# Performance work log

Hardware: AMD Instinct MI355X
Metric: run time of the kernel (lower is better)

The kernel has to match this reference:

```python
import jax, jax.numpy as jnp
import numpy as np

N = 4096      # number of nodes (tokens)
U = 128       # units (feature dim)
E = 131072    # number of edges (avg degree 32)


def _sage(x, src, dst, W_l, b_l, W_r):
    """PyG SAGEConv with mean aggregation.
    out = lin_l(mean_{j->i} x_j) + lin_r(x_i); lin_l has bias, lin_r does not.
    """
    n = x.shape[0]
    agg = jax.ops.segment_sum(x[src], dst, num_segments=n)
    deg = jax.ops.segment_sum(jnp.ones((src.shape[0],), x.dtype), dst, num_segments=n)
    agg = agg / jnp.maximum(deg, 1.0)[:, None]  # nodes w/o in-edges -> 0
    return agg @ W_l.T + b_l + x @ W_r.T


def setup_inputs() -> dict:
    key = jax.random.key(0)
    ks = jax.random.split(key, 20)
    s = 1.0 / np.sqrt(U)
    inp = {
        "x": jax.random.normal(ks[0], (N, U), jnp.float32),
        "edge_index": jax.random.randint(ks[1], (2, E), 0, N, jnp.int64),
        "batch": jnp.zeros((N,), jnp.int64),
        # conv_first
        "Wf_l": jax.random.normal(ks[2], (U, U), jnp.float32) * s,
        "bf_l": jnp.zeros((U,), jnp.float32),
        "Wf_r": jax.random.normal(ks[3], (U, U), jnp.float32) * s,
        # conv_common[0]
        "Wcm_l": jax.random.normal(ks[4], (U, U), jnp.float32) * s,
        "bcm_l": jnp.zeros((U,), jnp.float32),
        "Wcm_r": jax.random.normal(ks[5], (U, U), jnp.float32) * s,
        # conv_actor[0]
        "Wa_l": jax.random.normal(ks[6], (U, U), jnp.float32) * s,
        "ba_l": jnp.zeros((U,), jnp.float32),
        "Wa_r": jax.random.normal(ks[7], (U, U), jnp.float32) * s,
        # conv_critic[0]
        "Wcr_l": jax.random.normal(ks[8], (U, U), jnp.float32) * s,
        "bcr_l": jnp.zeros((U,), jnp.float32),
        "Wcr_r": jax.random.normal(ks[9], (U, U), jnp.float32) * s,
        # final_actor: Linear(2U, 1); final_critic: Linear(U, 1)
        "Wfa": jax.random.normal(ks[10], (1, 2 * U), jnp.float32) * (1.0 / np.sqrt(2 * U)),
        "bfa": jnp.zeros((1,), jnp.float32),
        "Wfc": jax.random.normal(ks[11], (1, U), jnp.float32) * s,
        "bfc": jnp.zeros((1,), jnp.float32),
    }
    return inp


def reference(x, edge_index, batch, Wf_l, bf_l, Wf_r, Wcm_l, bcm_l, Wcm_r,
              Wa_l, ba_l, Wa_r, Wcr_l, bcr_l, Wcr_r, Wfa, bfa, Wfc, bfc):
    src, dst = edge_index[0], edge_index[1]
    h = jnp.tanh(_sage(x, src, dst, Wf_l, bf_l, Wf_r))
    h = jnp.tanh(_sage(h, src, dst, Wcm_l, bcm_l, Wcm_r))

    # actor head: 1 SAGE layer (no activation since it is the last)
    x_actor = _sage(h, src, dst, Wa_l, ba_l, Wa_r)
    n = x_actor.shape[0]
    # pairwise row (i, j) feature = concat(x_actor[i], x_actor[j]) fed to Linear(2U,1).
    # Algebraically: score[i,j] = x_actor[i] @ w1 + x_actor[j] @ w2 + b  (same math,
    w1, w2 = Wfa[0, :U], Wfa[0, U:]
    scores = (x_actor @ w1)[:, None] + (x_actor @ w2)[None, :] + bfa[0]  # [N, N]
    edge_actor = jax.nn.log_softmax(scores.reshape(-1))[:, None]  # log_softmax over dim 0 of [N*N, 1]

    # critic head on detached features
    x_critic = _sage(jax.lax.stop_gradient(h), src, dst, Wcr_l, bcr_l, Wcr_r)
    cp = x_critic @ Wfc[0]  # [N]
    s = (cp[:, None] + cp[None, :]) * 0.5 + bfc[0]  # score[i,j] = ((c_i+c_j)/2) @ w + b
    edge_critic = jnp.tanh(jnp.mean(s)).reshape(1, 1)  # global_mean_pool over all N^2 rows
    return edge_actor, edge_critic
```

## Files before the change

kernel.cpp:

```cpp
#include <hip/hip_runtime.h>
#include <cstddef>

#define NN 4096
#define UF 128
#define NE 131072
#define SLOT_SHIFT 7
#define SLOTS (1 << SLOT_SHIFT)

typedef __attribute__((ext_vector_type(8))) short short8;
typedef __attribute__((ext_vector_type(4))) float f32x4;

__device__ __forceinline__ short f2bf(float f) {
  unsigned u = __float_as_uint(f);
  unsigned r = (u + 0x7fffu + ((u >> 16) & 1u)) >> 16;
  return (short)r;
}
__device__ __forceinline__ short8 cvt8(float4 w0, float4 w1) {
  short8 s;
  s[0] = f2bf(w0.x); s[1] = f2bf(w0.y); s[2] = f2bf(w0.z); s[3] = f2bf(w0.w);
  s[4] = f2bf(w1.x); s[5] = f2bf(w1.y); s[6] = f2bf(w1.z); s[7] = f2bf(w1.w);
  return s;
}

__device__ __forceinline__ int detect_is32(const void* ei) {
  const long long* e64 = (const long long*)ei;
  long long v = e64[threadIdx.x & 63];
  return (__ballot(v < 0 || v >= NN) != 0ull) ? 1 : 0;
}
__device__ __forceinline__ int edge_at(const void* ei, int is32, int idx) {
  if (is32) return ((const int*)ei)[idx];
  return (int)((const long long*)ei)[idx];
}

__global__ void k_scatter(const void* __restrict__ ei,
                          int* __restrict__ cnt, int* __restrict__ csr) {
  int is32 = detect_is32(ei);
  int e = blockIdx.x * blockDim.x + threadIdx.x;
  if (e >= NE) return;
  int s = edge_at(ei, is32, e);
  int d = edge_at(ei, is32, NE + e);
  int pos = atomicAdd(&cnt[d], 1);
  if (pos < SLOTS) csr[(d << SLOT_SHIFT) + pos] = s;
}

__device__ __forceinline__ void gather2(
    int base, const float* __restrict__ feat,
    const int* __restrict__ cnt, const int* __restrict__ csr,
    float (*As32)[132]) {
  const int t = threadIdx.x;
  const int lane = t & 63, wv = t >> 6;
  int nodeA = base + wv, nodeB = base + wv + 8;
  int nA = min(cnt[nodeA], SLOTS), nB = min(cnt[nodeB], SLOTS);
  int sA = nodeA << SLOT_SHIFT, sB = nodeB << SLOT_SHIFT;
  float ax0 = 0.f, ax1 = 0.f, ay0 = 0.f, ay1 = 0.f;
  float bx0 = 0.f, bx1 = 0.f, by0 = 0.f, by1 = 0.f;
  int iters = (max(nA, nB) + 7) >> 3;
  for (int it = 0; it < iters; ++it) {
    int e0 = it * 8;
    int idx[16];
#pragma unroll
    for (int j = 0; j < 8; ++j) { int ee = e0 + j; idx[j]     = csr[sA + (ee < nA ? ee : 0)]; }
#pragma unroll
    for (int j = 0; j < 8; ++j) { int ee = e0 + j; idx[8 + j] = csr[sB + (ee < nB ? ee : 0)]; }
#pragma unroll
    for (int j = 0; j < 16; ++j) { unsigned u = (unsigned)idx[j]; idx[j] = (u < NN) ? (int)u : 0; }
    float2 v[16];
#pragma unroll
    for (int j = 0; j < 16; ++j)
      v[j] = *((const float2*)(feat + (size_t)idx[j] * UF) + lane);
#pragma unroll
    for (int j = 0; j < 8; ++j) {
      bool ok = (e0 + j) < nA;
      if (j & 1) { ax1 += ok ? v[j].x : 0.f; ay1 += ok ? v[j].y : 0.f; }
      else       { ax0 += ok ? v[j].x : 0.f; ay0 += ok ? v[j].y : 0.f; }
    }
#pragma unroll
    for (int j = 0; j < 8; ++j) {
      bool ok = (e0 + j) < nB;
      if (j & 1) { bx1 += ok ? v[8+j].x : 0.f; by1 += ok ? v[8+j].y : 0.f; }
      else       { bx0 += ok ? v[8+j].x : 0.f; by0 += ok ? v[8+j].y : 0.f; }
    }
  }
  float invA = 1.0f / (float)max(nA, 1);
  float invB = 1.0f / (float)max(nB, 1);
  float2 rA; rA.x = (ax0 + ax1) * invA; rA.y = (ay0 + ay1) * invA;
  float2 rB; rB.x = (bx0 + bx1) * invB; rB.y = (by0 + by1) * invB;
  *(float2*)&As32[wv][2 * lane]     = rA;
  *(float2*)&As32[wv + 8][2 * lane] = rB;
}

__device__ __forceinline__ void repackA(
    int base, const float* __restrict__ feat,
    const float (*As32)[132], short (*AsF)[64][8]) {
  const int t = threadIdx.x;
  int kc = t >> 6, fl = t & 63;
  int row = fl & 15, ks = (fl >> 4) * 8;
  float f[8];
  if (kc < 4) {
    int k0 = kc * 32 + ks;
#pragma unroll
    for (int j = 0; j < 8; ++j) f[j] = As32[row][k0 + j];
  } else {
    const float* src = feat + (size_t)(base + row) * UF + (kc - 4) * 32 + ks;
    float4 w0 = *(const float4*)src, w1 = *(const float4*)(src + 4);
    f[0] = w0.x; f[1] = w0.y; f[2] = w0.z; f[3] = w0.w;
    f[4] = w1.x; f[5] = w1.y; f[6] = w1.z; f[7] = w1.w;
  }
  short8 av;
#pragma unroll
  for (int j = 0; j < 8; ++j) av[j] = f2bf(f[j]);
  *(short8*)&AsF[kc][fl][0] = av;
}

template<bool TANH>
__global__ __launch_bounds__(512, 4) void k_agglayer(
    const float* __restrict__ feat, const int* __restrict__ cnt,
    const int* __restrict__ csr,
    const float* __restrict__ Wl, const float* __restrict__ bl,
    const float* __restrict__ Wr, float* __restrict__ out) {
  __shared__ float As32[16][132];
  __shared__ short AsF[8][64][8];
  __shared__ short WsF[8][64][8];
  const int t = threadIdx.x;
  const int base = blockIdx.x * 16;
  const int lane = t & 63, w = t >> 6;

  gather2(base, feat, cnt, csr, As32);
  __syncthreads();
  repackA(base, feat, As32, AsF);

  f32x4 acc = {0.f, 0.f, 0.f, 0.f};
  for (int kc = 0; kc < 8; ++kc) {
    __syncthreads();
    {
      int o = w * 16 + (lane & 15);
      int ks = kc * 32 + (lane >> 4) * 8;
      const float* src = (ks < 128) ? (Wl + (size_t)o * UF + ks)
                                    : (Wr + (size_t)o * UF + (ks - 128));
      float4 w0 = *(const float4*)src, w1 = *(const float4*)(src + 4);
      *(short8*)&WsF[w][lane][0] = cvt8(w0, w1);
    }
    __syncthreads();
    short8 a = *(const short8*)&AsF[kc][lane][0];
    short8 b = *(const short8*)&WsF[w][lane][0];
    acc = __builtin_amdgcn_mfma_f32_16x16x32_bf16(a, b, acc, 0, 0, 0);
  }
  int col = lane & 15, rb = (lane >> 4) * 4;
  int o = w * 16 + col;
  float bias = bl[o];
#pragma unroll
  for (int r = 0; r < 4; ++r) {
    float v = acc[r] + bias;
    if (TANH) v = tanhf(v);
    out[(size_t)(base + rb + r) * UF + o] = v;
  }
}

__global__ __launch_bounds__(512, 4) void k_aggheads(
    const float* __restrict__ feat, const int* __restrict__ cnt,
    const int* __restrict__ csr,
    const float* __restrict__ Wa_l, const float* __restrict__ ba_l,
    const float* __restrict__ Wa_r,
    const float* __restrict__ Wcr_l, const float* __restrict__ bcr_l,
    const float* __restrict__ Wcr_r,
    const float* __restrict__ Wfa, const float* __restrict__ Wfc,
    float* __restrict__ a1, float* __restrict__ a2, float* __restrict__ sums) {
  __shared__ float As32[16][132];
  __shared__ short AsF[8][64][8];
  __shared__ short WsFA[8][64][8];
  __shared__ short WsFC[8][64][8];
  __shared__ float red[3][16][9];
  const int t = threadIdx.x;
  const int base = blockIdx.x * 16;
  const int lane = t & 63, w = t >> 6;

  gather2(base, feat, cnt, csr, As32);
  __syncthreads();
  repackA(base, feat, As32, AsF);

  f32x4 accA = {0.f, 0.f, 0.f, 0.f};
  f32x4 accC = {0.f, 0.f, 0.f, 0.f};
  for (int kc = 0; kc < 8; ++kc) {
    __syncthreads();
    {
      int o = w * 16 + (lane & 15);
      int ks = kc * 32 + (lane >> 4) * 8;
      const float* sA = (ks < 128) ? (Wa_l  + (size_t)o * UF + ks)
                                   : (Wa_r  + (size_t)o * UF + (ks - 128));
      const float* sC = (ks < 128) ? (Wcr_l + (size_t)o * UF + ks)
                                   : (Wcr_r + (size_t)o * UF + (ks - 128));
      float4 a0 = *(const float4*)sA, a1v = *(const float4*)(sA + 4);
      float4 c0 = *(const float4*)sC, c1v = *(const float4*)(sC + 4);
      *(short8*)&WsFA[w][lane][0] = cvt8(a0, a1v);
      *(short8*)&WsFC[w][lane][0] = cvt8(c0, c1v);
    }
    __syncthreads();
    short8 a  = *(const short8*)&AsF[kc][lane][0];
    short8 ba = *(const short8*)&WsFA[w][lane][0];
    short8 bc = *(const short8*)&WsFC[w][lane][0];
    accA = __builtin_amdgcn_mfma_f32_16x16x32_bf16(a, ba, accA, 0, 0, 0);
    accC = __builtin_amdgcn_mfma_f32_16x16x32_bf16(a, bc, accC, 0, 0, 0);
  }
  int col = lane & 15, rb = (lane >> 4) * 4;
  int o = w * 16 + col;
  float baA = ba_l[o], baC = bcr_l[o];
  float w1 = Wfa[o], w2 = Wfa[UF + o], wfc = Wfc[o];
  float p1[4], p2[4], pc[4];
#pragma unroll
  for (int r = 0; r < 4; ++r) {
    float xa = accA[r] + baA;
    float xc = accC[r] + baC;
    p1[r] = xa * w1; p2[r] = xa * w2; pc[r] = xc * wfc;
  }
#pragma unroll
  for (int d = 1; d < 16; d <<= 1) {
#pragma unroll
    for (int r = 0; r < 4; ++r) {
      p1[r] += __shfl_xor(p1[r], d, 64);
      p2[r] += __shfl_xor(p2[r], d, 64);
      pc[r] += __shfl_xor(pc[r], d, 64);
    }
  }
  if (col == 0) {
#pragma unroll
    for (int r = 0; r < 4; ++r) {
      red[0][rb + r][w] = p1[r];
      red[1][rb + r][w] = p2[r];
      red[2][rb + r][w] = pc[r];
    }
  }
  __syncthreads();
  if (t < 48) {
    int q = t >> 4, n = t & 15;
    float s = 0.f;
#pragma unroll
    for (int j = 0; j < 8; ++j) s += red[q][n][j];
    if (q == 0) a1[base + n] = s;
    else if (q == 1) a2[base + n] = s;
    float v = (q < 2) ? expf(s) : s;
#pragma unroll
    for (int d = 1; d < 16; d <<= 1) v += __shfl_xor(v, d, 64);
    if ((t & 15) == 0) atomicAdd(&sums[q], v);
  }
}

__global__ __launch_bounds__(256) void k_write(
    const float* __restrict__ a1, const float* __restrict__ a2,
    const float* __restrict__ sums, const float* __restrict__ bfc,
    float* __restrict__ out) {
  const int t = blockIdx.x * 256 + threadIdx.x;
  const int lane = threadIdx.x & 63;
  float C = 0.f;
  if (lane == 0) C = -(logf(sums[0]) + logf(sums[1]));
  C = __shfl(C, 0, 64);
#pragma unroll
  for (int k = 0; k < 8; ++k) {
    int gid = t + k * 524288;
    int row = gid >> 10;
    int c = (gid & 1023) * 4;
    float Cr = C + a1[row];
    float4 v = *(const float4*)(a2 + c);
    float4 r; r.x = v.x + Cr; r.y = v.y + Cr; r.z = v.z + Cr; r.w = v.w + Cr;
    *(float4*)(out + (size_t)gid * 4) = r;
  }
  if (t == 0)
    out[(size_t)NN * NN] = tanhf(sums[2] * (1.0f / (float)NN) + bfc[0]);
}

extern "C" void kernel_launch(void* const* d_in, const int* in_sizes, int n_in,
                              void* d_out, int out_size, void* d_ws, size_t ws_size,
                              hipStream_t stream) {
  const float* x     = (const float*)d_in[0];
  const void*  ei    = d_in[1];
  const float* Wf_l  = (const float*)d_in[3];
  const float* bf_l  = (const float*)d_in[4];
  const float* Wf_r  = (const float*)d_in[5];
  const float* Wcm_l = (const float*)d_in[6];
  const float* bcm_l = (const float*)d_in[7];
  const float* Wcm_r = (const float*)d_in[8];
  const float* Wa_l  = (const float*)d_in[9];
  const float* ba_l  = (const float*)d_in[10];
  const float* Wa_r  = (const float*)d_in[11];
  const float* Wcr_l = (const float*)d_in[12];
  const float* bcr_l = (const float*)d_in[13];
  const float* Wcr_r = (const float*)d_in[14];
  const float* Wfa   = (const float*)d_in[15];
  const float* Wfc   = (const float*)d_in[17];
  const float* bfc   = (const float*)d_in[18];
  float* out = (float*)d_out;

  char* b = (char*)d_ws;
  size_t off = 0;
  float* sums = (float*)(b + off); off += 512;
  int* cnt = (int*)(b + off); off += (size_t)NN * 4;
  int* csr = (int*)(b + off); off += (size_t)NN * SLOTS * 4;
  float* a1 = (float*)(b + off); off += (size_t)NN * 4;
  float* a2 = (float*)(b + off); off += (size_t)NN * 4;
  float* h1 = (float*)(b + off); off += (size_t)NN * UF * 4;
  float* h2 = (float*)(b + off); off += (size_t)NN * UF * 4;
  if (ws_size < off) return;

  hipMemsetAsync(d_ws, 0, 512 + (size_t)NN * 4, stream);
  k_scatter<<<NE / 256, 256, 0, stream>>>(ei, cnt, csr);
  k_agglayer<true><<<NN / 16, 512, 0, stream>>>(x,  cnt, csr, Wf_l,  bf_l,  Wf_r,  h1);
  k_agglayer<true><<<NN / 16, 512, 0, stream>>>(h1, cnt, csr, Wcm_l, bcm_l, Wcm_r, h2);
  k_aggheads<<<NN / 16, 512, 0, stream>>>(h2, cnt, csr, Wa_l, ba_l, Wa_r,
                                          Wcr_l, bcr_l, Wcr_r, Wfa, Wfc, a1, a2, sums);
  k_write<<<2048, 256, 0, stream>>>(a1, a2, sums, bfc, out);
}
```

Before: 93.30 us.

## Store hidden activations in bf16 and feed MFMA operands directly from registers

The intermediate hidden features h1 and h2 are now stored as bf16 instead of fp32, which halves the bytes moved by the edge gathers in the second layer and the heads layer. The shared-memory repack of A and W operands and the per-k-chunk __syncthreads are removed. Each lane now converts its A fragment from the aggregation buffer (or from the node's own features) and loads W straight from global memory into MFMA operands. Launch bounds drop to 2 blocks per SM. The risks are extra bf16 rounding on activations and more redundant global weight loads.

```diff
diff --git a/kernel.cpp b/kernel.cpp
--- a/kernel.cpp
+++ b/kernel.cpp
@@ -9,11 +9,15 @@
 
 typedef __attribute__((ext_vector_type(8))) short short8;
 typedef __attribute__((ext_vector_type(4))) float f32x4;
+typedef unsigned short bf16_t;
 
 __device__ __forceinline__ short f2bf(float f) {
   unsigned u = __float_as_uint(f);
   unsigned r = (u + 0x7fffu + ((u >> 16) & 1u)) >> 16;
   return (short)r;
+}
+__device__ __forceinline__ float bf2f(unsigned short u) {
+  return __uint_as_float(((unsigned)u) << 16);
 }
 __device__ __forceinline__ short8 cvt8(float4 w0, float4 w1) {
   short8 s;
@@ -30,6 +34,26 @@
 __device__ __forceinline__ int edge_at(const void* ei, int is32, int idx) {
   if (is32) return ((const int*)ei)[idx];
   return (int)((const long long*)ei)[idx];
+}
+
+__device__ __forceinline__ float2 ld_row(const float* feat, int row, int lane) {
+  return *((const float2*)(feat + (size_t)row * UF) + lane);
+}
+__device__ __forceinline__ float2 ld_row(const bf16_t* feat, int row, int lane) {
+  ushort2 u = *((const ushort2*)(feat + (size_t)row * UF) + lane);
+  float2 f; f.x = bf2f(u.x); f.y = bf2f(u.y); return f;
+}
+__device__ __forceinline__ short8 load_own(const float* feat, int row, int kk) {
+  const float* src = feat + (size_t)row * UF + kk;
+  float4 a0 = *(const float4*)src, a1 = *(const float4*)(src + 4);
+  return cvt8(a0, a1);
+}
+__device__ __forceinline__ short8 load_own(const bf16_t* feat, int row, int kk) {
+  return *(const short8*)(feat + (size_t)row * UF + kk);
+}
+__device__ __forceinline__ void store_out(float* p, size_t i, float v) { p[i] = v; }
+__device__ __forceinline__ void store_out(bf16_t* p, size_t i, float v) {
+  p[i] = (bf16_t)f2bf(v);
 }
 
 __global__ void k_scatter(const void* __restrict__ ei,
@@ -43,10 +67,11 @@
   if (pos < SLOTS) csr[(d << SLOT_SHIFT) + pos] = s;
 }
 
+template<typename T>
 __device__ __forceinline__ void gather2(
-    int base, const float* __restrict__ feat,
+    int base, const T* __restrict__ feat,
     const int* __restrict__ cnt, const int* __restrict__ csr,
-    float (*As32)[132]) {
+    float (*As32)[140]) {
   const int t = threadIdx.x;
   const int lane = t & 63, wv = t >> 6;
   int nodeA = base + wv, nodeB = base + wv + 8;
@@ -66,8 +91,7 @@
     for (int j = 0; j < 16; ++j) { unsigned u = (unsigned)idx[j]; idx[j] = (u < NN) ? (int)u : 0; }
     float2 v[16];
 #pragma unroll
-    for (int j = 0; j < 16; ++j)
-      v[j] = *((const float2*)(feat + (size_t)idx[j] * UF) + lane);
+    for (int j = 0; j < 16; ++j) v[j] = ld_row(feat, idx[j], lane);
 #pragma unroll
     for (int j = 0; j < 8; ++j) {
       bool ok = (e0 + j) < nA;
@@ -89,75 +113,53 @@
   *(float2*)&As32[wv + 8][2 * lane] = rB;
 }
 
-__device__ __forceinline__ void repackA(
-    int base, const float* __restrict__ feat,
-    const float (*As32)[132], short (*AsF)[64][8]) {
-  const int t = threadIdx.x;
-  int kc = t >> 6, fl = t & 63;
-  int row = fl & 15, ks = (fl >> 4) * 8;
-  float f[8];
-  if (kc < 4) {
-    int k0 = kc * 32 + ks;
-#pragma unroll
-    for (int j = 0; j < 8; ++j) f[j] = As32[row][k0 + j];
-  } else {
-    const float* src = feat + (size_t)(base + row) * UF + (kc - 4) * 32 + ks;
-    float4 w0 = *(const float4*)src, w1 = *(const float4*)(src + 4);
-    f[0] = w0.x; f[1] = w0.y; f[2] = w0.z; f[3] = w0.w;
-    f[4] = w1.x; f[5] = w1.y; f[6] = w1.z; f[7] = w1.w;
-  }
-  short8 av;
-#pragma unroll
-  for (int j = 0; j < 8; ++j) av[j] = f2bf(f[j]);
-  *(short8*)&AsF[kc][fl][0] = av;
-}
-
-template<bool TANH>
-__global__ __launch_bounds__(512, 4) void k_agglayer(
-    const float* __restrict__ feat, const int* __restrict__ cnt,
+template<bool TANH, typename TIN, typename TOUT>
+__global__ __launch_bounds__(512, 2) void k_agglayer(
+    const TIN* __restrict__ feat, const int* __restrict__ cnt,
     const int* __restrict__ csr,
     const float* __restrict__ Wl, const float* __restrict__ bl,
-    const float* __restrict__ Wr, float* __restrict__ out) {
-  __shared__ float As32[16][132];
-  __shared__ short AsF[8][64][8];
-  __shared__ short WsF[8][64][8];
+    const float* __restrict__ Wr, TOUT* __restrict__ out) {
+  __shared__ float As32[16][140];
   const int t = threadIdx.x;
   const int base = blockIdx.x * 16;
   const int lane = t & 63, w = t >> 6;
 
   gather2(base, feat, cnt, csr, As32);
   __syncthreads();
-  repackA(base, feat, As32, AsF);
-
+
+  const int row = lane & 15;
+  const int ks8 = (lane >> 4) * 8;
+  const int o = w * 16 + row;
   f32x4 acc = {0.f, 0.f, 0.f, 0.f};
+#pragma unroll
   for (int kc = 0; kc < 8; ++kc) {
-    __syncthreads();
-    {
-      int o = w * 16 + (lane & 15);
-      int ks = kc * 32 + (lane >> 4) * 8;
-      const float* src = (ks < 128) ? (Wl + (size_t)o * UF + ks)
-                                    : (Wr + (size_t)o * UF + (ks - 128));
-      float4 w0 = *(const float4*)src, w1 = *(const float4*)(src + 4);
-      *(short8*)&WsF[w][lane][0] = cvt8(w0, w1);
-    }
-    __syncthreads();
-    short8 a = *(const short8*)&AsF[kc][lane][0];
-    short8 b = *(const short8*)&WsF[w][lane][0];
+    short8 a;
+    if (kc < 4) {
+      const float* pa = &As32[row][kc * 32 + ks8];
+      float4 a0 = *(const float4*)pa, a1 = *(const float4*)(pa + 4);
+      a = cvt8(a0, a1);
+    } else {
+      a = load_own(feat, base + row, (kc - 4) * 32 + ks8);
+    }
+    int kg = kc * 32 + ks8;
+    const float* ws = (kg < 128) ? (Wl + (size_t)o * UF + kg)
+                                 : (Wr + (size_t)o * UF + (kg - 128));
+    float4 w0 = *(const float4*)ws, w1 = *(const float4*)(ws + 4);
+    short8 b = cvt8(w0, w1);
     acc = __builtin_amdgcn_mfma_f32_16x16x32_bf16(a, b, acc, 0, 0, 0);
   }
-  int col = lane & 15, rb = (lane >> 4) * 4;
-  int o = w * 16 + col;
+  int rb = (lane >> 4) * 4;
   float bias = bl[o];
 #pragma unroll
   for (int r = 0; r < 4; ++r) {
     float v = acc[r] + bias;
     if (TANH) v = tanhf(v);
-    out[(size_t)(base + rb + r) * UF + o] = v;
-  }
-}
-
-__global__ __launch_bounds__(512, 4) void k_aggheads(
-    const float* __restrict__ feat, const int* __restrict__ cnt,
+    store_out(out, (size_t)(base + rb + r) * UF + o, v);
+  }
+}
+
+__global__ __launch_bounds__(512, 2) void k_aggheads(
+    const bf16_t* __restrict__ feat, const int* __restrict__ cnt,
     const int* __restrict__ csr,
     const float* __restrict__ Wa_l, const float* __restrict__ ba_l,
     const float* __restrict__ Wa_r,
@@ -165,10 +167,7 @@
     const float* __restrict__ Wcr_r,
     const float* __restrict__ Wfa, const float* __restrict__ Wfc,
     float* __restrict__ a1, float* __restrict__ a2, float* __restrict__ sums) {
-  __shared__ float As32[16][132];
-  __shared__ short AsF[8][64][8];
-  __shared__ short WsFA[8][64][8];
-  __shared__ short WsFC[8][64][8];
+  __shared__ float As32[16][140];
   __shared__ float red[3][16][9];
   const int t = threadIdx.x;
   const int base = blockIdx.x * 16;
@@ -176,33 +175,35 @@
 
   gather2(base, feat, cnt, csr, As32);
   __syncthreads();
-  repackA(base, feat, As32, AsF);
-
+
+  const int row = lane & 15;
+  const int ks8 = (lane >> 4) * 8;
+  const int o = w * 16 + row;
   f32x4 accA = {0.f, 0.f, 0.f, 0.f};
   f32x4 accC = {0.f, 0.f, 0.f, 0.f};
+#pragma unroll
   for (int kc = 0; kc < 8; ++kc) {
-    __syncthreads();
-    {
-      int o = w * 16 + (lane & 15);
-      int ks = kc * 32 + (lane >> 4) * 8;
-      const float* sA = (ks < 128) ? (Wa_l  + (size_t)o * UF + ks)
-                                   : (Wa_r  + (size_t)o * UF + (ks - 128));
-      const float* sC = (ks < 128) ? (Wcr_l + (size_t)o * UF + ks)
-                                   : (Wcr_r + (size_t)o * UF + (ks - 128));
-      float4 a0 = *(const float4*)sA, a1v = *(const float4*)(sA + 4);
-      float4 c0 = *(const float4*)sC, c1v = *(const float4*)(sC + 4);
-      *(short8*)&WsFA[w][lane][0] = cvt8(a0, a1v);
-      *(short8*)&WsFC[w][lane][0] = cvt8(c0, c1v);
-    }
-    __syncthreads();
-    short8 a  = *(const short8*)&AsF[kc][lane][0];
-    short8 ba = *(const short8*)&WsFA[w][lane][0];
-    short8 bc = *(const short8*)&WsFC[w][lane][0];
+    short8 a;
+    if (kc < 4) {
+      const float* pa = &As32[row][kc * 32 + ks8];
+      float4 a0 = *(const float4*)pa, a1v = *(const float4*)(pa + 4);
+      a = cvt8(a0, a1v);
+    } else {
+      a = load_own(feat, base + row, (kc - 4) * 32 + ks8);
+    }
+    int kg = kc * 32 + ks8;
+    const float* sA = (kg < 128) ? (Wa_l  + (size_t)o * UF + kg)
+                                 : (Wa_r  + (size_t)o * UF + (kg - 128));
+    const float* sC = (kg < 128) ? (Wcr_l + (size_t)o * UF + kg)
+                                 : (Wcr_r + (size_t)o * UF + (kg - 128));
+    float4 wa0 = *(const float4*)sA, wa1 = *(const float4*)(sA + 4);
+    float4 wc0 = *(const float4*)sC, wc1 = *(const float4*)(sC + 4);
+    short8 ba = cvt8(wa0, wa1);
+    short8 bc = cvt8(wc0, wc1);
     accA = __builtin_amdgcn_mfma_f32_16x16x32_bf16(a, ba, accA, 0, 0, 0);
     accC = __builtin_amdgcn_mfma_f32_16x16x32_bf16(a, bc, accC, 0, 0, 0);
   }
   int col = lane & 15, rb = (lane >> 4) * 4;
-  int o = w * 16 + col;
   float baA = ba_l[o], baC = bcr_l[o];
   float w1 = Wfa[o], w2 = Wfa[UF + o], wfc = Wfc[o];
   float p1[4], p2[4], pc[4];
@@ -296,14 +297,16 @@
   int* csr = (int*)(b + off); off += (size_t)NN * SLOTS * 4;
   float* a1 = (float*)(b + off); off += (size_t)NN * 4;
   float* a2 = (float*)(b + off); off += (size_t)NN * 4;
-  float* h1 = (float*)(b + off); off += (size_t)NN * UF * 4;
-  float* h2 = (float*)(b + off); off += (size_t)NN * UF * 4;
+  bf16_t* h1 = (bf16_t*)(b + off); off += (size_t)NN * UF * 2;
+  bf16_t* h2 = (bf16_t*)(b + off); off += (size_t)NN * UF * 2;
   if (ws_size < off) return;
 
   hipMemsetAsync(d_ws, 0, 512 + (size_t)NN * 4, stream);
   k_scatter<<<NE / 256, 256, 0, stream>>>(ei, cnt, csr);
-  k_agglayer<true><<<NN / 16, 512, 0, stream>>>(x,  cnt, csr, Wf_l,  bf_l,  Wf_r,  h1);
-  k_agglayer<true><<<NN / 16, 512, 0, stream>>>(h1, cnt, csr, Wcm_l, bcm_l, Wcm_r, h2);
+  k_agglayer<true, float,  bf16_t><<<NN / 16, 512, 0, stream>>>(
+      x,  cnt, csr, Wf_l,  bf_l,  Wf_r,  h1);
+  k_agglayer<true, bf16_t, bf16_t><<<NN / 16, 512, 0, stream>>>(
+      h1, cnt, csr, Wcm_l, bcm_l, Wcm_r, h2);
   k_aggheads<<<NN / 16, 512, 0, stream>>>(h2, cnt, csr, Wa_l, ba_l, Wa_r,
                                           Wcr_l, bcr_l, Wcr_r, Wfa, Wfc, a1, a2, sums);
   k_write<<<2048, 256, 0, stream>>>(a1, a2, sums, bfc, out);
```

After: 86.35 us. 7.5% less time.
